# Optimization experiments

Measured on AMD Instinct MI355X. Metric: run time of the kernel, lower is better.

The kernel has to match this reference:

```python
import jax, jax.numpy as jnp
import numpy as np
from jax import lax

DIM = 512
H = 8
WIN = 32            # local_window_size
TEMP = 1.0          # softmax temperature
PTEMP = 0.5         # pattern temperature
SPARSITY = 0.3      # sparsity_ratio default in create_learned_sparse_mask
THRESH = 0.1


def setup_inputs() -> dict:
    key = jax.random.key(0)
    ks = jax.random.split(key, 10)
    B, L, D = 4, 1024, DIM

    def w(k, shape, std=0.02):
        return jax.random.normal(k, shape, jnp.float32) * std

    return {
        "x": jax.random.normal(ks[0], (B, L, D), jnp.float32),
        "mask": jnp.ones((B, L), jnp.int32),
        "qkv_w": w(ks[1], (3 * D, D)),
        "proj_w": w(ks[2], (D, D)),
        "proj_b": jnp.zeros((D,), jnp.float32),
        "ps_w1": w(ks[3], (D, D)),
        "ps_b1": jnp.zeros((D,), jnp.float32),
        "ps_w2": w(ks[4], (D // 2, D)),
        "ps_b2": jnp.zeros((D // 2,), jnp.float32),
        "ps_w3": w(ks[5], (3, D // 2)),
        "ps_b3": jnp.array([0.5, -0.5, 0.0], jnp.float32),
        "pattern_bias": jnp.array([0.2, -0.1, -0.1], jnp.float32),
        "sparse_w": jax.random.normal(ks[6], (H,), jnp.float32) * 0.2,
        "sparse_b": jnp.zeros((H,), jnp.float32),
    }


def reference(x, mask, qkv_w, proj_w, proj_b, ps_w1, ps_b1, ps_w2, ps_b2,
              ps_w3, ps_b3, pattern_bias, sparse_w, sparse_b):
    B, L, D = x.shape
    hd = D // H
    scale = hd ** -0.5

    # qkv projection -> (3, B, H, L, hd)
    qkv = (x @ qkv_w.T).reshape(B, L, 3, H, hd).transpose(2, 0, 3, 1, 4)
    q, k, v = qkv[0], qkv[1], qkv[2]
    scores = jnp.einsum('bhqd,bhkd->bhqk', q, k) * scale  # (B,H,L,L)

    # pattern selector on mean-pooled features (enhanced path is skipped: D+1 != D)
    pooled = x.mean(axis=1)
    h1 = jax.nn.relu(pooled @ ps_w1.T + ps_b1)
    h2 = jax.nn.relu(h1 @ ps_w2.T + ps_b2)
    logits = h2 @ ps_w3.T + ps_b3 + pattern_bias  # (B,3)
    pw = jax.nn.softmax(logits / PTEMP, axis=-1)

    # local mask: row i attends to [i-half, i+half]
    half = WIN // 2
    idx = jnp.arange(L)
    local = (jnp.abs(idx[:, None] - idx[None, :]) <= half).astype(jnp.float32)

    # learned sparse mask via per-head affine + jitter + top-k scatter (no grad)
    kk = max(1, min(L, int(L * (1 - SPARSITY))))
    s = lax.stop_gradient(scores) * sparse_w[None, :, None, None] + sparse_b[None, :, None, None]
    jitter = jax.random.normal(jax.random.key(42), s.shape, jnp.float32) * 1e-6
    _, top_idx = lax.top_k(s + jitter, kk)  # (B,H,L,kk)
    bi = jnp.arange(B)[:, None, None, None]
    hi = jnp.arange(H)[None, :, None, None]
    li = jnp.arange(L)[None, None, :, None]
    sparse = jnp.zeros((B, H, L, L), jnp.float32).at[bi, hi, li, top_idx].set(1.0)

    combined = (pw[:, 0, None, None, None] * local
                + pw[:, 1, None, None, None]
                + pw[:, 2, None, None, None] * sparse)
    allow = combined > THRESH

    neg_inf = -jnp.inf
    scores = jnp.where(allow, scores, neg_inf)

    # padding key mask (1 = keep); guard fully-padded rows like the original
    mask_fixed = mask.at[:, 0].set(jnp.where(mask.sum(axis=1) == 0, 1, mask[:, 0]))
    scores = jnp.where(mask_fixed[:, None, None, :] != 0, scores, neg_inf)

    # rows that are entirely -inf: unmask position 0 with score 0
    all_masked = jnp.all(jnp.isneginf(scores), axis=-1)  # (B,H,L)
    scores = jnp.where(all_masked[..., None] & (idx == 0), 0.0, scores)

    attn = jax.nn.softmax(scores / TEMP, axis=-1)
    out = jnp.einsum('bhqk,bhkd->bhqd', attn, v)
    out = out.transpose(0, 2, 1, 3).reshape(B, L, D)
    return out @ proj_w.T + proj_b
```

## Files before the change

### kernel.cpp

```cpp
#include <hip/hip_runtime.h>
#include <math.h>

#define NB   4
#define NH   8
#define SEQ  1024
#define DM   512
#define HD   64
#define WANT 715
#define ROWS 8

typedef float v2f __attribute__((ext_vector_type(2)));
__device__ __forceinline__ v2f mkv2(float a, float b){ v2f r; r.x=a; r.y=b; return r; }

#define OFF_Q    0u
#define OFF_KT   2097152u
#define OFF_VT   4194304u
#define OFF_AO   6291456u
#define OFF_PART 8388608u
#define OFF_CMB  8404992u
#define OFF_MSUM 8405008u
#define OFF_JIT  8405504u
#define WS_NEED_BYTES ((size_t)(OFF_JIT + 33554432u) * 4u)


__device__ __forceinline__ unsigned rotl32(unsigned x, int r){ return (x<<r)|(x>>(32-r)); }

__device__ __forceinline__ uint2 threefry_0_42(unsigned x0, unsigned x1){
  const unsigned ks0=0u, ks1=42u, ks2=0x1BD11BDAu^42u;
  x0+=ks0; x1+=ks1;
#define TFR(r) { x0+=x1; x1=rotl32(x1,(r)); x1^=x0; }
  TFR(13) TFR(15) TFR(26) TFR(6)
  x0+=ks1; x1+=ks2+1u;
  TFR(17) TFR(29) TFR(16) TFR(24)
  x0+=ks2; x1+=ks0+2u;
  TFR(13) TFR(15) TFR(26) TFR(6)
  x0+=ks0; x1+=ks1+3u;
  TFR(17) TFR(29) TFR(16) TFR(24)
  x0+=ks1; x1+=ks2+4u;
  TFR(13) TFR(15) TFR(26) TFR(6)
  x0+=ks2; x1+=ks0+5u;
#undef TFR
  return make_uint2(x0,x1);
}

__device__ __forceinline__ float erfinv_xla(float x){
  float w = -__logf(fmaf(-x, x, 1.0f));
  float p;
  if (w < 5.0f) {
    w -= 2.5f;
    p = 2.81022636e-08f;
    p = fmaf(p,w, 3.43273939e-07f);
    p = fmaf(p,w,-3.5233877e-06f);
    p = fmaf(p,w,-4.39150654e-06f);
    p = fmaf(p,w, 0.00021858087f);
    p = fmaf(p,w,-0.00125372503f);
    p = fmaf(p,w,-0.00417768164f);
    p = fmaf(p,w, 0.246640727f);
    p = fmaf(p,w, 1.50140941f);
  } else {
    w = sqrtf(w) - 3.0f;
    p = -0.000200214257f;
    p = fmaf(p,w, 0.000100950558f);
    p = fmaf(p,w, 0.00134934322f);
    p = fmaf(p,w,-0.00367342844f);
    p = fmaf(p,w, 0.00573950773f);
    p = fmaf(p,w,-0.0076224613f);
    p = fmaf(p,w, 0.00943887047f);
    p = fmaf(p,w, 1.00167406f);
    p = fmaf(p,w, 2.83297682f);
  }
  return p*x;
}

__device__ __forceinline__ float norm_from_bits(unsigned bits){
  float fl = __uint_as_float((bits >> 9) | 0x3F800000u) - 1.0f;
  float u  = fmaf(fl, 2.0f, -0.99999994f);
  u = fmaxf(-0.99999994f, u);
  return (1.41421356f * erfinv_xla(u)) * 1e-6f;
}

__device__ __forceinline__ float jitter_val(unsigned f){
  unsigned i   = f & 0xFFFFFFu;
  unsigned sel = f >> 24;
  uint2 rr = threefry_0_42(i, i + 0x1000000u);
  return norm_from_bits(sel ? rr.y : rr.x);
}

__global__ __launch_bounds__(256) void k_jit(float* __restrict__ jit){
  unsigned i = blockIdx.x*256u + threadIdx.x;
  uint2 rr = threefry_0_42(i, i + 0x1000000u);
  jit[i]              = norm_from_bits(rr.x);
  jit[i + 0x1000000u] = norm_from_bits(rr.y);
}

__global__ __launch_bounds__(512) void k_pool(const float* __restrict__ x, float* __restrict__ part) {
  int b = blockIdx.x, ch = blockIdx.y, c = threadIdx.x;
  const float* xp = x + ((size_t)(b*SEQ + ch*128))*DM + c;
  float s = 0.f;
  for (int l=0;l<128;l++) s += xp[(size_t)l*DM];
  part[(b*8+ch)*DM + c] = s;
}

__global__ __launch_bounds__(512) void k_pattern(const float* __restrict__ part, const int* __restrict__ mask,
    const float* __restrict__ w1, const float* __restrict__ b1,
    const float* __restrict__ w2, const float* __restrict__ b2,
    const float* __restrict__ w3, const float* __restrict__ b3,
    const float* __restrict__ pbias, float* __restrict__ cmb, int* __restrict__ msum) {
  __shared__ __align__(16) float pooled[DM];
  __shared__ __align__(16) float h1[DM];
  __shared__ __align__(16) float h2[DM/2];
  __shared__ float lg[3];
  __shared__ int msum_s;
  int b = blockIdx.x, t = threadIdx.x;
  float p = 0.f;
  for (int ch=0; ch<8; ++ch) p += part[(b*8+ch)*DM + t];
  pooled[t] = p * (1.0f/1024.0f);
  if (t == 0) msum_s = 0;
  __syncthreads();
  atomicAdd(&msum_s, mask[b*SEQ + t] + mask[b*SEQ + 512 + t]);
  {
    float a = 0.f; const float4* wr = (const float4*)(w1 + (size_t)t*DM);
    const float4* pp = (const float4*)pooled;
    for (int c4=0;c4<DM/4;c4++) {
      float4 wv4 = wr[c4], pv4 = pp[c4];
      a += wv4.x*pv4.x; a += wv4.y*pv4.y; a += wv4.z*pv4.z; a += wv4.w*pv4.w;
    }
    a += b1[t];
    h1[t] = fmaxf(a, 0.f);
  }
  __syncthreads();
  if (t < 256) {
    float a = 0.f; const float4* wr = (const float4*)(w2 + (size_t)t*DM);
    const float4* hh = (const float4*)h1;
    for (int c4=0;c4<DM/4;c4++) {
      float4 wv4 = wr[c4], hv4 = hh[c4];
      a += wv4.x*hv4.x; a += wv4.y*hv4.y; a += wv4.z*hv4.z; a += wv4.w*hv4.w;
    }
    a += b2[t];
    h2[t] = fmaxf(a, 0.f);
  }
  __syncthreads();
  if (t < 3) {
    float a = 0.f; const float4* wr = (const float4*)(w3 + t*256);
    const float4* hh = (const float4*)h2;
    for (int c4=0;c4<64;c4++) {
      float4 wv4 = wr[c4], hv4 = hh[c4];
      a += wv4.x*hv4.x; a += wv4.y*hv4.y; a += wv4.z*hv4.z; a += wv4.w*hv4.w;
    }
    a += b3[t] + pbias[t];
    lg[t] = a * 2.0f;
  }
  __syncthreads();
  if (t == 0) {
    float m = fmaxf(lg[0], fmaxf(lg[1], lg[2]));
    float e0 = expf(lg[0]-m), e1 = expf(lg[1]-m), e2 = expf(lg[2]-m);
    float Z = e0+e1+e2;
    float pw0 = e0/Z, pw1 = e1/Z, pw2 = e2/Z;
    cmb[b*4+0] = pw1;
    cmb[b*4+1] = pw0 + pw1;
    cmb[b*4+2] = pw1 + pw2;
    cmb[b*4+3] = (pw0 + pw1) + pw2;
    msum[b] = msum_s;
  }
}

__global__ __launch_bounds__(256) void k_qkv(const float* __restrict__ x, const float* __restrict__ w,
                                             float* __restrict__ ws) {
  __shared__ __align__(16) float As[32][128];
  __shared__ __align__(16) float Bs[32][64];
  int tid = threadIdx.x;
  int bm = blockIdx.x, bn = blockIdx.y;
  int ty = tid >> 4, tx = tid & 15;
  v2f acc2[8][2];
  #pragma unroll
  for (int i=0;i<8;i++) { acc2[i][0] = mkv2(0.f,0.f); acc2[i][1] = mkv2(0.f,0.f); }
  for (int kt=0; kt<16; ++kt) {
    #pragma unroll
    for (int q4=0;q4<4;q4++) {
      int f = tid*4+q4; int row = f>>3; int cc = (f&7)*4;
      float4 ga = *(const float4*)&x[(size_t)(bm*128+row)*DM + kt*32 + cc];
      As[cc+0][row]=ga.x; As[cc+1][row]=ga.y; As[cc+2][row]=ga.z; As[cc+3][row]=ga.w;
    }
    #pragma unroll
    for (int q4=0;q4<2;q4++) {
      int f = tid*2+q4; int row = f>>3; int cc = (f&7)*4;
      float4 gb = *(const float4*)&w[(size_t)(bn*64+row)*DM + kt*32 + cc];
      Bs[cc+0][row]=gb.x; Bs[cc+1][row]=gb.y; Bs[cc+2][row]=gb.z; Bs[cc+3][row]=gb.w;
    }
    __syncthreads();
    #pragma unroll
    for (int kk=0;kk<32;kk++) {
      float4 a0 = *(const float4*)&As[kk][ty*8];
      float4 a1 = *(const float4*)&As[kk][ty*8+4];
      float4 b4 = *(const float4*)&Bs[kk][tx*4];
      float av[8] = {a0.x,a0.y,a0.z,a0.w,a1.x,a1.y,a1.z,a1.w};
      v2f b01 = mkv2(b4.x,b4.y), b23 = mkv2(b4.z,b4.w);
      #pragma unroll
      for (int i=0;i<8;i++) {
        v2f s = mkv2(av[i], av[i]);
        acc2[i][0] = __builtin_elementwise_fma(s, b01, acc2[i][0]);
        acc2[i][1] = __builtin_elementwise_fma(s, b23, acc2[i][1]);
      }
    }
    __syncthreads();
  }
  float acc[8][4];
  #pragma unroll
  for (int i=0;i<8;i++) {
    acc[i][0]=acc2[i][0].x; acc[i][1]=acc2[i][0].y;
    acc[i][2]=acc2[i][1].x; acc[i][3]=acc2[i][1].y;
  }
  int m0 = bn*64;
  int s = m0 >> 9;
  int h = (m0 >> 6) & 7;
  int b = bm >> 3;
  int l0 = (bm & 7) * 128;
  int d0 = tx*4;
  if (s == 0) {
    #pragma unroll
    for (int i=0;i<8;i++) {
      int l = l0 + ty*8 + i;
      float4 o = {acc[i][0],acc[i][1],acc[i][2],acc[i][3]};
      *(float4*)&ws[OFF_Q + ((size_t)((b*NH+h)*SEQ + l))*HD + d0] = o;
    }
  } else {
    unsigned off = (s == 1) ? OFF_KT : OFF_VT;
    size_t base = off + ((size_t)((b*NH+h)*HD))*SEQ;
    #pragma unroll
    for (int j=0;j<4;j++) {
      float4 c0 = {acc[0][j], acc[1][j], acc[2][j], acc[3][j]};
      float4 c1 = {acc[4][j], acc[5][j], acc[6][j], acc[7][j]};
      size_t cb = base + (size_t)(d0+j)*SEQ + l0 + ty*8;
      *(float4*)&ws[cb]     = c0;
      *(float4*)&ws[cb + 4] = c1;
    }
  }
}

template<int USEJIT>
__global__ __launch_bounds__(256, 4) void k_attn(
    const float* __restrict__ ws_q, const float* __restrict__ ws_kT, const float* __restrict__ ws_vT,
    const int* __restrict__ mask, const float* __restrict__ cmb, const int* __restrict__ msum,
    const float* __restrict__ sparse_w, const float* __restrict__ sparse_b,
    const float* __restrict__ jit, float* __restrict__ ao) {
  __shared__ __align__(16) float pbuf[ROWS][SEQ];
  __shared__ __align__(16) float q_s[ROWS][HD];
  __shared__ float mxred[4][ROWS], smred[4][ROWS];
  __shared__ unsigned pfx_s[ROWS];
  __shared__ int want_s[ROWS];
  __shared__ float mxrow[ROWS], rowsum[ROWS];
  __shared__ float cmb_s[4];

  unsigned* hist = (unsigned*)&pbuf[0][0];
  float (*red)[ROWS][HD] = (float (*)[ROWS][HD])&pbuf[0][0];

  int tid = threadIdx.x;
  int gid = blockIdx.x;
  int bh = gid >> 7;
  int rt = gid & 127;
  int b = bh >> 3, h = bh & 7;
  int qbase = rt * ROWS;

  {
    const float* qp = ws_q + ((size_t)bh*SEQ + qbase)*HD;
    if (tid < 128) ((float4*)q_s)[tid] = ((const float4*)qp)[tid];
    if (tid < 4) cmb_s[tid] = cmb[b*4+tid];
    if (tid < ROWS) { pfx_s[tid] = 0u; want_s[tid] = WANT; }
  }
  __syncthreads();

  float score[4][ROWS];
  {
    const float* kT = ws_kT + (size_t)bh*HD*SEQ;
    #pragma unroll
    for (int c=0;c<4;c++)
      #pragma unroll
      for (int r=0;r<ROWS;r++) score[c][r]=0.f;
    for (int d4=0; d4<16; ++d4) {
      float4 qv[ROWS];
      #pragma unroll
      for (int r=0;r<ROWS;r++) qv[r] = *(const float4*)&q_s[r][d4*4];
      float4 ka = *(const float4*)&kT[(size_t)(d4*4+0)*SEQ + tid*4];
      float4 kb = *(const float4*)&kT[(size_t)(d4*4+1)*SEQ + tid*4];
      float4 kc = *(const float4*)&kT[(size_t)(d4*4+2)*SEQ + tid*4];
      float4 kd = *(const float4*)&kT[(size_t)(d4*4+3)*SEQ + tid*4];
      #pragma unroll
      for (int r=0;r<ROWS;r++) {
        score[0][r] += qv[r].x*ka.x + qv[r].y*kb.x + qv[r].z*kc.x + qv[r].w*kd.x;
        score[1][r] += qv[r].x*ka.y + qv[r].y*kb.y + qv[r].z*kc.y + qv[r].w*kd.y;
        score[2][r] += qv[r].x*ka.z + qv[r].y*kb.z + qv[r].z*kc.z + qv[r].w*kd.z;
        score[3][r] += qv[r].x*ka.w + qv[r].y*kb.w + qv[r].z*kc.w + qv[r].w*kd.w;
      }
    }
    #pragma unroll
    for (int c=0;c<4;c++)
      #pragma unroll
      for (int r=0;r<ROWS;r++)
        score[c][r] *= 0.125f;
  }

  unsigned u[4][ROWS];
  {
    float sw = sparse_w[h], sb = sparse_b[h];
    #pragma unroll
    for (int r=0;r<ROWS;r++) {
      unsigned fbase = ((unsigned)bh << 20) + ((unsigned)(qbase + r) << 10);
      float jv[4];
      if (USEJIT) {
        float4 j4 = *(const float4*)&jit[fbase + (unsigned)(tid*4)];
        jv[0]=j4.x; jv[1]=j4.y; jv[2]=j4.z; jv[3]=j4.w;
      } else {
        #pragma unroll
        for (int c=0;c<4;c++) jv[c] = jitter_val(fbase + (unsigned)(tid*4+c));
      }
      #pragma unroll
      for (int c=0;c<4;c++) {
        float s = score[c][r]*sw + sb + jv[c];
        unsigned bu = __float_as_uint(s);
        u[c][r] = (bu & 0x80000000u) ? ~bu : (bu | 0x80000000u);
      }
    }
  }

  {
    int r2 = tid >> 5, w = tid & 31;
    for (int pass=0; pass<4; ++pass) {
      int shift = 24 - 8*pass;
      for (int e = tid; e < ROWS*256; e += 256) hist[e] = 0u;
      __syncthreads();
      if (pass == 0) {
        #pragma unroll
        for (int r=0;r<ROWS;r++) {
          unsigned a = u[0][r] >> 24, bb = u[1][r] >> 24,
                   cc = u[2][r] >> 24, dd = u[3][r] >> 24;
          if (a == bb && a == cc && a == dd) {
            atomicAdd(&hist[r*256 + a], 4u);
          } else {
            atomicAdd(&hist[r*256 + a], 1u);
            atomicAdd(&hist[r*256 + bb], 1u);
            atomicAdd(&hist[r*256 + cc], 1u);
            atomicAdd(&hist[r*256 + dd], 1u);
          }
        }
      } else {
        unsigned hmask = 0xFFFFFFFFu << (shift+8);
        #pragma unroll
        for (int r=0;r<ROWS;r++) {
          unsigned pf = pfx_s[r];
          #pragma unroll
          for (int c=0;c<4;c++) {
            unsigned uu = u[c][r];
            if ((uu & hmask) == pf) atomicAdd(&hist[r*256 + ((uu>>shift)&255u)], 1u);
          }
        }
      }
      __syncthreads();
      unsigned cs = 0;
      #pragma unroll
      for (int k=0;k<8;k++) cs += hist[r2*256 + w*8 + k];
      unsigned is = cs;
      #pragma unroll
      for (int off=1; off<32; off<<=1) {
        unsigned tt = __shfl_down(is, off, 32);
        if (w + off < 32) is += tt;
      }
      unsigned es = is - cs;
      int want = want_s[r2];
      if ((int)es <= want && want < (int)(es + cs)) {
        int cacc = (int)es;
        for (int k=7;k>=0;k--) {
          unsigned hc = hist[r2*256 + w*8 + k];
          if (want < cacc + (int)hc) {
            pfx_s[r2] |= ((unsigned)(w*8+k)) << shift;
            want_s[r2] = want - cacc;
            break;
          }
          cacc += (int)hc;
        }
      }
      __syncthreads();
    }
  }

  unsigned spmask = 0u;
  {
    #pragma unroll
    for (int r=0;r<ROWS;r++) {
      unsigned Tr = pfx_s[r];
      #pragma unroll
      for (int c=0;c<4;c++)
        if (u[c][r] >= Tr) spmask |= 1u << (r*4+c);
    }
  }

  {
    float c00 = cmb_s[0], c10 = cmb_s[1], c01 = cmb_s[2], c11 = cmb_s[3];
    int msum_b = msum[b];
    const int4 m4 = *(const int4*)&mask[b*SEQ + tid*4];
    int mv[4] = {m4.x, m4.y, m4.z, m4.w};
    bool okm[4];
    #pragma unroll
    for (int c=0;c<4;c++) {
      int j = tid*4 + c;
      okm[c] = (mv[c] != 0) || (msum_b == 0 && j == 0);
    }
    float lmax[ROWS];
    #pragma unroll
    for (int r=0;r<ROWS;r++) {
      int qr = qbase + r;
      float lm = -INFINITY;
      #pragma unroll
      for (int c=0;c<4;c++) {
        int j = tid*4 + c;
        bool sp = (spmask >> (r*4+c)) & 1u;
        int dj = j - qr; dj = dj < 0 ? -dj : dj;
        float comb = (dj <= 16) ? (sp ? c11 : c10) : (sp ? c01 : c00);
        float val = (comb > 0.1f && okm[c]) ? score[c][r] : -INFINITY;
        score[c][r] = val;
        lm = fmaxf(lm, val);
      }
      lmax[r] = lm;
    }
    #pragma unroll
    for (int r=0;r<ROWS;r++)
      #pragma unroll
      for (int off=32; off>=1; off>>=1)
        lmax[r] = fmaxf(lmax[r], __shfl_xor(lmax[r], off, 64));
    int wv = tid >> 6, lane = tid & 63;
    if (lane == 0) {
      #pragma unroll
      for (int r=0;r<ROWS;r++) mxred[wv][r] = lmax[r];
    }
    __syncthreads();
    if (tid < ROWS)
      mxrow[tid] = fmaxf(fmaxf(mxred[0][tid], mxred[1][tid]), fmaxf(mxred[2][tid], mxred[3][tid]));
    __syncthreads();
    float lsum[ROWS];
    #pragma unroll
    for (int r=0;r<ROWS;r++) {
      float M = mxrow[r];
      bool allm = (M == -INFINITY);
      float p0, p1, p2, p3;
      if (allm) {
        p0 = (tid == 0) ? 1.0f : 0.0f; p1 = 0.f; p2 = 0.f; p3 = 0.f;
      } else {
        p0 = __expf(score[0][r] - M);
        p1 = __expf(score[1][r] - M);
        p2 = __expf(score[2][r] - M);
        p3 = __expf(score[3][r] - M);
      }
      float4 pv = {p0,p1,p2,p3};
      *(float4*)&pbuf[r][tid*4] = pv;
      lsum[r] = p0+p1+p2+p3;
    }
    #pragma unroll
    for (int r=0;r<ROWS;r++)
      #pragma unroll
      for (int off=32; off>=1; off>>=1)
        lsum[r] += __shfl_xor(lsum[r], off, 64);
    if (lane == 0) {
      #pragma unroll
      for (int r=0;r<ROWS;r++) smred[wv][r] = lsum[r];
    }
    __syncthreads();
    if (tid < ROWS)
      rowsum[tid] = smred[0][tid] + smred[1][tid] + smred[2][tid] + smred[3][tid];
  }
  __syncthreads();

  {
    int wv = tid >> 6, l = tid & 63;
    const float* vt = ws_vT + ((size_t)bh*HD + l)*SEQ;
    v2f acc2[ROWS];
    #pragma unroll
    for (int r=0;r<ROWS;r++) acc2[r] = mkv2(0.f,0.f);
    int jb = wv*256;
    for (int j8=0;j8<32;j8++) {
      int j = jb + j8*8;
      float4 va = *(const float4*)&vt[j];
      float4 vb = *(const float4*)&vt[j+4];
      v2f va01 = mkv2(va.x,va.y), va23 = mkv2(va.z,va.w);
      v2f vb01 = mkv2(vb.x,vb.y), vb23 = mkv2(vb.z,vb.w);
      #pragma unroll
      for (int r=0;r<ROWS;r++) {
        float4 pa = *(const float4*)&pbuf[r][j];
        float4 pb = *(const float4*)&pbuf[r][j+4];
        v2f t = acc2[r];
        t = __builtin_elementwise_fma(mkv2(pa.x,pa.y), va01, t);
        t = __builtin_elementwise_fma(mkv2(pa.z,pa.w), va23, t);
        t = __builtin_elementwise_fma(mkv2(pb.x,pb.y), vb01, t);
        t = __builtin_elementwise_fma(mkv2(pb.z,pb.w), vb23, t);
        acc2[r] = t;
      }
    }
    float acc[ROWS];
    #pragma unroll
    for (int r=0;r<ROWS;r++) acc[r] = acc2[r].x + acc2[r].y;
    __syncthreads();
    if (wv > 0) {
      #pragma unroll
      for (int r=0;r<ROWS;r++) red[wv-1][r][l] = acc[r];
    }
    __syncthreads();
    if (wv == 0) {
      #pragma unroll
      for (int r=0;r<ROWS;r++) {
        float tot = acc[r] + red[0][r][l] + red[1][r][l] + red[2][r][l];
        ao[((size_t)(b*SEQ + qbase + r))*DM + h*HD + l] = tot / rowsum[r];
      }
    }
  }
}

__global__ __launch_bounds__(256) void k_proj(const float* __restrict__ aoin, const float* __restrict__ w,
                                              const float* __restrict__ bias, float* __restrict__ out) {
  __shared__ __align__(16) float As[32][128];
  __shared__ __align__(16) float Bs[32][64];
  int tid = threadIdx.x;
  int bm = blockIdx.x, bn = blockIdx.y;
  int ty = tid >> 4, tx = tid & 15;
  v2f acc2[8][2];
  #pragma unroll
  for (int i=0;i<8;i++) { acc2[i][0] = mkv2(0.f,0.f); acc2[i][1] = mkv2(0.f,0.f); }
  for (int kt=0; kt<16; ++kt) {
    #pragma unroll
    for (int q4=0;q4<4;q4++) {
      int f = tid*4+q4; int row = f>>3; int cc = (f&7)*4;
      float4 ga = *(const float4*)&aoin[(size_t)(bm*128+row)*DM + kt*32 + cc];
      As[cc+0][row]=ga.x; As[cc+1][row]=ga.y; As[cc+2][row]=ga.z; As[cc+3][row]=ga.w;
    }
    #pragma unroll
    for (int q4=0;q4<2;q4++) {
      int f = tid*2+q4; int row = f>>3; int cc = (f&7)*4;
      float4 gb = *(const float4*)&w[(size_t)(bn*64+row)*DM + kt*32 + cc];
      Bs[cc+0][row]=gb.x; Bs[cc+1][row]=gb.y; Bs[cc+2][row]=gb.z; Bs[cc+3][row]=gb.w;
    }
    __syncthreads();
    #pragma unroll
    for (int kk=0;kk<32;kk++) {
      float4 a0 = *(const float4*)&As[kk][ty*8];
      float4 a1 = *(const float4*)&As[kk][ty*8+4];
      float4 b4 = *(const float4*)&Bs[kk][tx*4];
      float av[8] = {a0.x,a0.y,a0.z,a0.w,a1.x,a1.y,a1.z,a1.w};
      v2f b01 = mkv2(b4.x,b4.y), b23 = mkv2(b4.z,b4.w);
      #pragma unroll
      for (int i=0;i<8;i++) {
        v2f s = mkv2(av[i], av[i]);
        acc2[i][0] = __builtin_elementwise_fma(s, b01, acc2[i][0]);
        acc2[i][1] = __builtin_elementwise_fma(s, b23, acc2[i][1]);
      }
    }
    __syncthreads();
  }
  int o0 = bn*64 + tx*4;
  float4 bvv = *(const float4*)&bias[o0];
  #pragma unroll
  for (int i=0;i<8;i++) {
    int tok = bm*128 + ty*8 + i;
    float4 o;
    o.x = acc2[i][0].x + bvv.x; o.y = acc2[i][0].y + bvv.y;
    o.z = acc2[i][1].x + bvv.z; o.w = acc2[i][1].y + bvv.w;
    *(float4*)&out[(size_t)tok*DM + o0] = o;
  }
}

extern "C" void kernel_launch(void* const* d_in, const int* in_sizes, int n_in,
                              void* d_out, int out_size, void* d_ws, size_t ws_size,
                              hipStream_t stream) {
  const float* x        = (const float*)d_in[0];
  const int*   mask     = (const int*)  d_in[1];
  const float* qkv_w    = (const float*)d_in[2];
  const float* proj_w   = (const float*)d_in[3];
  const float* proj_b   = (const float*)d_in[4];
  const float* ps_w1    = (const float*)d_in[5];
  const float* ps_b1    = (const float*)d_in[6];
  const float* ps_w2    = (const float*)d_in[7];
  const float* ps_b2    = (const float*)d_in[8];
  const float* ps_w3    = (const float*)d_in[9];
  const float* ps_b3    = (const float*)d_in[10];
  const float* pbias    = (const float*)d_in[11];
  const float* sparse_w = (const float*)d_in[12];
  const float* sparse_b = (const float*)d_in[13];
  float* ws  = (float*)d_ws;
  float* out = (float*)d_out;

  const bool use_jit = (ws_size >= WS_NEED_BYTES);

  k_pool<<<dim3(NB,8), 512, 0, stream>>>(x, ws + OFF_PART);
  k_pattern<<<NB, 512, 0, stream>>>(ws + OFF_PART, mask, ps_w1, ps_b1, ps_w2, ps_b2,
                                    ps_w3, ps_b3, pbias, ws + OFF_CMB, (int*)(ws + OFF_MSUM));
  if (use_jit) k_jit<<<65536, 256, 0, stream>>>(ws + OFF_JIT);
  k_qkv<<<dim3(32,24), 256, 0, stream>>>(x, qkv_w, ws);
  if (use_jit) {
    k_attn<1><<<NB*NH*(SEQ/ROWS), 256, 0, stream>>>(ws + OFF_Q, ws + OFF_KT, ws + OFF_VT, mask,
                                                    ws + OFF_CMB, (const int*)(ws + OFF_MSUM),
                                                    sparse_w, sparse_b, ws + OFF_JIT, ws + OFF_AO);
  } else {
    k_attn<0><<<NB*NH*(SEQ/ROWS), 256, 0, stream>>>(ws + OFF_Q, ws + OFF_KT, ws + OFF_VT, mask,
                                                    ws + OFF_CMB, (const int*)(ws + OFF_MSUM),
                                                    sparse_w, sparse_b, ws + OFF_JIT, ws + OFF_AO);
  }
  k_proj<<<dim3(32,8), 256, 0, stream>>>(ws + OFF_AO, proj_w, proj_b, out);
}
```

Before: 457.8 us.

## Merge jitter generation into QKV kernel and store V row-major

The separate jitter-generation kernel is folded into the QKV GEMM launch as extra blocks, so the two overlap and one launch is saved. V is now written row-major (L×HD) instead of transposed. In the attention kernel, each thread reads V with a strided scalar load per key, which is coalesced across lanes, in place of the earlier float4 loads along the transposed layout. The per-thread access becomes eight scalar loads instead of two vector loads, which may change load efficiency.

```diff
diff --git a/kernel.cpp b/kernel.cpp
--- a/kernel.cpp
+++ b/kernel.cpp
@@ -14,7 +14,7 @@
 
 #define OFF_Q    0u
 #define OFF_KT   2097152u
-#define OFF_VT   4194304u
+#define OFF_V    4194304u
 #define OFF_AO   6291456u
 #define OFF_PART 8388608u
 #define OFF_CMB  8404992u
@@ -86,13 +86,6 @@
   return norm_from_bits(sel ? rr.y : rr.x);
 }
 
-__global__ __launch_bounds__(256) void k_jit(float* __restrict__ jit){
-  unsigned i = blockIdx.x*256u + threadIdx.x;
-  uint2 rr = threefry_0_42(i, i + 0x1000000u);
-  jit[i]              = norm_from_bits(rr.x);
-  jit[i + 0x1000000u] = norm_from_bits(rr.y);
-}
-
 __global__ __launch_bounds__(512) void k_pool(const float* __restrict__ x, float* __restrict__ part) {
   int b = blockIdx.x, ch = blockIdx.y, c = threadIdx.x;
   const float* xp = x + ((size_t)(b*SEQ + ch*128))*DM + c;
@@ -164,12 +157,19 @@
   }
 }
 
-__global__ __launch_bounds__(256) void k_qkv(const float* __restrict__ x, const float* __restrict__ w,
-                                             float* __restrict__ ws) {
+__global__ __launch_bounds__(256) void k_qkv_jit(const float* __restrict__ x, const float* __restrict__ w,
+                                                 float* __restrict__ ws, float* __restrict__ jit) {
   __shared__ __align__(16) float As[32][128];
   __shared__ __align__(16) float Bs[32][64];
   int tid = threadIdx.x;
-  int bm = blockIdx.x, bn = blockIdx.y;
+  if (blockIdx.x >= 768) {
+    unsigned i = (blockIdx.x - 768u)*256u + tid;
+    uint2 rr = threefry_0_42(i, i + 0x1000000u);
+    jit[i]              = norm_from_bits(rr.x);
+    jit[i + 0x1000000u] = norm_from_bits(rr.y);
+    return;
+  }
+  int bm = blockIdx.x & 31, bn = blockIdx.x >> 5;
   int ty = tid >> 4, tx = tid & 15;
   v2f acc2[8][2];
   #pragma unroll
@@ -216,16 +216,16 @@
   int b = bm >> 3;
   int l0 = (bm & 7) * 128;
   int d0 = tx*4;
-  if (s == 0) {
+  if (s == 0 || s == 2) {
+    unsigned off = (s == 0) ? OFF_Q : OFF_V;
     #pragma unroll
     for (int i=0;i<8;i++) {
       int l = l0 + ty*8 + i;
       float4 o = {acc[i][0],acc[i][1],acc[i][2],acc[i][3]};
-      *(float4*)&ws[OFF_Q + ((size_t)((b*NH+h)*SEQ + l))*HD + d0] = o;
+      *(float4*)&ws[off + ((size_t)((b*NH+h)*SEQ + l))*HD + d0] = o;
     }
   } else {
-    unsigned off = (s == 1) ? OFF_KT : OFF_VT;
-    size_t base = off + ((size_t)((b*NH+h)*HD))*SEQ;
+    size_t base = OFF_KT + ((size_t)((b*NH+h)*HD))*SEQ;
     #pragma unroll
     for (int j=0;j<4;j++) {
       float4 c0 = {acc[0][j], acc[1][j], acc[2][j], acc[3][j]};
@@ -239,7 +239,7 @@
 
 template<int USEJIT>
 __global__ __launch_bounds__(256, 4) void k_attn(
-    const float* __restrict__ ws_q, const float* __restrict__ ws_kT, const float* __restrict__ ws_vT,
+    const float* __restrict__ ws_q, const float* __restrict__ ws_kT, const float* __restrict__ ws_v,
     const int* __restrict__ mask, const float* __restrict__ cmb, const int* __restrict__ msum,
     const float* __restrict__ sparse_w, const float* __restrict__ sparse_b,
     const float* __restrict__ jit, float* __restrict__ ao) {
@@ -470,17 +470,24 @@
 
   {
     int wv = tid >> 6, l = tid & 63;
-    const float* vt = ws_vT + ((size_t)bh*HD + l)*SEQ;
+    const float* vrow = ws_v + ((size_t)bh*SEQ)*HD + l;
+    float acc[ROWS];
     v2f acc2[ROWS];
     #pragma unroll
     for (int r=0;r<ROWS;r++) acc2[r] = mkv2(0.f,0.f);
     int jb = wv*256;
     for (int j8=0;j8<32;j8++) {
       int j = jb + j8*8;
-      float4 va = *(const float4*)&vt[j];
-      float4 vb = *(const float4*)&vt[j+4];
-      v2f va01 = mkv2(va.x,va.y), va23 = mkv2(va.z,va.w);
-      v2f vb01 = mkv2(vb.x,vb.y), vb23 = mkv2(vb.z,vb.w);
+      float v0 = vrow[(size_t)(j+0)*HD];
+      float v1 = vrow[(size_t)(j+1)*HD];
+      float v2 = vrow[(size_t)(j+2)*HD];
+      float v3 = vrow[(size_t)(j+3)*HD];
+      float v4 = vrow[(size_t)(j+4)*HD];
+      float v5 = vrow[(size_t)(j+5)*HD];
+      float v6 = vrow[(size_t)(j+6)*HD];
+      float v7 = vrow[(size_t)(j+7)*HD];
+      v2f va01 = mkv2(v0,v1), va23 = mkv2(v2,v3);
+      v2f vb01 = mkv2(v4,v5), vb23 = mkv2(v6,v7);
       #pragma unroll
       for (int r=0;r<ROWS;r++) {
         float4 pa = *(const float4*)&pbuf[r][j];
@@ -493,7 +500,6 @@
         acc2[r] = t;
       }
     }
-    float acc[ROWS];
     #pragma unroll
     for (int r=0;r<ROWS;r++) acc[r] = acc2[r].x + acc2[r].y;
     __syncthreads();
@@ -589,14 +595,13 @@
   k_pool<<<dim3(NB,8), 512, 0, stream>>>(x, ws + OFF_PART);
   k_pattern<<<NB, 512, 0, stream>>>(ws + OFF_PART, mask, ps_w1, ps_b1, ps_w2, ps_b2,
                                     ps_w3, ps_b3, pbias, ws + OFF_CMB, (int*)(ws + OFF_MSUM));
-  if (use_jit) k_jit<<<65536, 256, 0, stream>>>(ws + OFF_JIT);
-  k_qkv<<<dim3(32,24), 256, 0, stream>>>(x, qkv_w, ws);
+  k_qkv_jit<<<use_jit ? 66304 : 768, 256, 0, stream>>>(x, qkv_w, ws, ws + OFF_JIT);
   if (use_jit) {
-    k_attn<1><<<NB*NH*(SEQ/ROWS), 256, 0, stream>>>(ws + OFF_Q, ws + OFF_KT, ws + OFF_VT, mask,
+    k_attn<1><<<NB*NH*(SEQ/ROWS), 256, 0, stream>>>(ws + OFF_Q, ws + OFF_KT, ws + OFF_V, mask,
                                                     ws + OFF_CMB, (const int*)(ws + OFF_MSUM),
                                                     sparse_w, sparse_b, ws + OFF_JIT, ws + OFF_AO);
   } else {
-    k_attn<0><<<NB*NH*(SEQ/ROWS), 256, 0, stream>>>(ws + OFF_Q, ws + OFF_KT, ws + OFF_VT, mask,
+    k_attn<0><<<NB*NH*(SEQ/ROWS), 256, 0, stream>>>(ws + OFF_Q, ws + OFF_KT, ws + OFF_V, mask,
                                                     ws + OFF_CMB, (const int*)(ws + OFF_MSUM),
                                                     sparse_w, sparse_b, ws + OFF_JIT, ws + OFF_AO);
   }
```

After: 430.3 us. -6.0%, faster.
